# Kernel tuning notes

Measured on AMD Instinct MI355X. Metric: run time of the kernel, lower is better.

## Reference

```python
import jax, jax.numpy as jnp
import numpy as np

N, T, DS, DD = 20000, 8, 16, 8   # nodes, seq_len, static dim, dynamic dim
E = 320000                        # edges (before self loops)
HL = 128                          # LSTM hidden
GH, GC = 4, 128                   # GAT heads, channels per head
HC = GH * GC                      # 512 concat output
EMB = 64
IN1 = DS + HL                     # layer-1 GNN input dim (static + lstm)


def setup_inputs() -> dict:
    ks = jax.random.split(jax.random.key(0), 20)
    p = lambda k, s: jax.random.normal(k, s, jnp.float32) * 0.05
    return {
        "x_static": jax.random.normal(ks[0], (N, DS), jnp.float32),
        "dynamic_seq": jax.random.normal(ks[1], (N, T, DD), jnp.float32),
        "edge_index": jax.random.randint(ks[2], (2, E), 0, N),
        # LSTM params (PyTorch gate order i,f,g,o)
        "W_ih": p(ks[3], (4 * HL, DD)), "W_hh": p(ks[4], (4 * HL, HL)),
        "b_ih": p(ks[5], (4 * HL,)), "b_hh": p(ks[6], (4 * HL,)),
        # GATv2 layer 1
        "Wl1": p(ks[7], (HC, IN1)), "Wr1": p(ks[8], (HC, IN1)),
        "att1": p(ks[9], (GH, GC)), "bg1": p(ks[10], (HC,)),
        # GATv2 layer 2
        "Wl2": p(ks[11], (HC, HC)), "Wr2": p(ks[12], (HC, HC)),
        "att2": p(ks[13], (GH, GC)), "bg2": p(ks[14], (HC,)),
        # BatchNorm affine params
        "gamma1": jnp.ones((HC,), jnp.float32), "beta1": jnp.zeros((HC,), jnp.float32),
        "gamma2": jnp.ones((HC,), jnp.float32), "beta2": jnp.zeros((HC,), jnp.float32),
        # output projection
        "Wp": p(ks[15], (EMB, HC)), "bp": p(ks[16], (EMB,)),
    }


def _lstm(seq, W_ih, W_hh, b_ih, b_hh):
    """Single-layer LSTM over [N, T, DD] -> [T, N, HL]."""
    n = seq.shape[0]
    b = b_ih + b_hh

    def step(carry, x_t):
        h, c = carry
        g = x_t @ W_ih.T + h @ W_hh.T + b            # [N, 4*HL]
        i, f, gg, o = jnp.split(g, 4, axis=-1)
        c = jax.nn.sigmoid(f) * c + jax.nn.sigmoid(i) * jnp.tanh(gg)
        h = jax.nn.sigmoid(o) * jnp.tanh(c)
        return (h, c), h

    h0 = jnp.zeros((n, HL), seq.dtype)
    _, hs = jax.lax.scan(step, (h0, h0), jnp.swapaxes(seq, 0, 1))
    return hs


def _gatv2(x, src, dst, Wl, Wr, att, bias):
    """GATv2Conv (concat heads, self-loops already in src/dst, eval dropout)."""
    xl = (x @ Wl.T).reshape(N, GH, GC)   # source transform
    xr = (x @ Wr.T).reshape(N, GH, GC)   # target transform
    e = jax.nn.leaky_relu(xl[src] + xr[dst], 0.2)       # [E', GH, GC]
    s = jnp.einsum('ehc,hc->eh', e, att)                # [E', GH]
    smax = jax.ops.segment_max(s, dst, num_segments=N)  # scatter-softmax (stable)
    ex = jnp.exp(s - smax[dst])
    den = jax.ops.segment_sum(ex, dst, num_segments=N)
    alpha = ex / den[dst]
    out = jax.ops.segment_sum(alpha[:, :, None] * xl[src], dst, num_segments=N)
    return out.reshape(N, HC) + bias


def _bn(x, g, b):
    m = x.mean(0)
    v = x.var(0)
    return (x - m) * jax.lax.rsqrt(v + 1e-5) * g + b


def reference(x_static, dynamic_seq, edge_index, W_ih, W_hh, b_ih, b_hh,
              Wl1, Wr1, att1, bg1, Wl2, Wr2, att2, bg2,
              gamma1, beta1, gamma2, beta2, Wp, bp):
    loops = jnp.arange(N)
    src = jnp.concatenate([edge_index[0], loops])  # add self loops (PyG default)
    dst = jnp.concatenate([edge_index[1], loops])
    hs = _lstm(dynamic_seq, W_ih, W_hh, b_ih, b_hh)  # [T, N, HL]

    def step(_, h_t):
        g = jnp.concatenate([x_static, h_t], axis=1)                 # [N, IN1]
        g = jax.nn.relu(_bn(_gatv2(g, src, dst, Wl1, Wr1, att1, bg1), gamma1, beta1))
        g = jax.nn.relu(_bn(_gatv2(g, src, dst, Wl2, Wr2, att2, bg2), gamma2, beta2))
        return None, g @ Wp.T + bp                                   # [N, EMB]

    _, emb = jax.lax.scan(step, None, hs)  # [T, N, EMB]
    return jnp.swapaxes(emb, 0, 1)         # [N, T, EMB]
```

## Files before the change

### kernel.cpp

```cpp
#include <hip/hip_runtime.h>
#include <math.h>

typedef unsigned short u16;
typedef unsigned int u32;

#define N_NODES 20000
#define MP      20480
#define T_SEQ   8
#define DS      16
#define DD      8
#define E_EDGES 320000
#define HL      128
#define GH      4
#define GC      128
#define HC      512
#define EMB     64
#define KP1     160
#define EP      (E_EDGES + N_NODES)
#define EPP     (EP + 3 * N_NODES)

typedef __attribute__((ext_vector_type(8))) short bf16x8;
typedef __attribute__((ext_vector_type(4))) float f32x4;

__device__ __forceinline__ u16 f2bf(float f) {
  u32 u = __float_as_uint(f);
  u += 0x7fff + ((u >> 16) & 1);
  return (u16)(u >> 16);
}
__device__ __forceinline__ float bflo(u32 v) { return __uint_as_float(v << 16); }
__device__ __forceinline__ float bfhi(u32 v) { return __uint_as_float(v & 0xffff0000u); }
__device__ __forceinline__ float bf16f(u16 v) { return __uint_as_float((u32)v << 16); }

__device__ __forceinline__ void gld16(const void* g, void* l) {
  __builtin_amdgcn_global_load_lds(
      (const __attribute__((address_space(1))) void*)g,
      (__attribute__((address_space(3))) void*)l, 16, 0, 0);
}

__device__ __forceinline__ float rowsum16(float p) {
  p += __int_as_float(__builtin_amdgcn_update_dpp(0, __float_as_int(p), 0x121, 0xf, 0xf, false));
  p += __int_as_float(__builtin_amdgcn_update_dpp(0, __float_as_int(p), 0x122, 0xf, 0xf, false));
  p += __int_as_float(__builtin_amdgcn_update_dpp(0, __float_as_int(p), 0x124, 0xf, 0xf, false));
  p += __int_as_float(__builtin_amdgcn_update_dpp(0, __float_as_int(p), 0x128, 0xf, 0xf, false));
  return p;
}

__global__ __launch_bounds__(256) void gemm_mfma(
    const u16* __restrict__ A, int lda,
    const u16* __restrict__ W, int ldw,
    const float* __restrict__ bias,
    void* __restrict__ Cout, int ldc,
    int M, int Nc, int K, int c_bf16, int gxs)
{
  __shared__ u16 smem[16384];
  u16* Asm = smem;
  u16* Bsm = smem + 8192;

  const int tid = threadIdx.x;
  const int wave = tid >> 6, lane = tid & 63;
  const int wm = (wave >> 1) << 6, wn = (wave & 1) << 6;

  const u32 id = blockIdx.x;
  const int xcd = id & 7;
  const u32 sl = id >> 3;
  const int GXm = (1 << gxs) - 1;
  const int bn = (int)(sl & GXm) << 7;
  const int bm = (xcd + (int)((sl >> gxs) << 3)) << 7;

  f32x4 acc[4][4];
#pragma unroll
  for (int i = 0; i < 4; ++i)
#pragma unroll
    for (int j = 0; j < 4; ++j) acc[i][j] = (f32x4){0.f, 0.f, 0.f, 0.f};

  const int qr = lane >> 2;
  const int qc = (lane & 3) << 3;
  const int q0 = wave * 2, q1 = wave * 2 + 1;
  const int ra0 = bm + q0 * 16 + qr;
  const int ra1 = bm + q1 * 16 + qr;
  int rb0 = bn + q0 * 16 + qr; if (rb0 >= Nc) rb0 = Nc - 1;
  int rb1 = bn + q1 * 16 + qr; if (rb1 >= Nc) rb1 = Nc - 1;

  const u16* pa0 = A + (size_t)ra0 * lda + qc;
  const u16* pa1 = A + (size_t)ra1 * lda + qc;
  const u16* pb0 = W + (size_t)rb0 * ldw + qc;
  const u16* pb1 = W + (size_t)rb1 * ldw + qc;

  const int fm = lane & 15;
  const int fk = (lane >> 4) << 3;

  gld16(pa0, &Asm[q0 * 512]);
  gld16(pa1, &Asm[q1 * 512]);
  gld16(pb0, &Bsm[q0 * 512]);
  gld16(pb1, &Bsm[q1 * 512]);
  pa0 += 32; pa1 += 32; pb0 += 32; pb1 += 32;

  const int iters = K >> 5;
#pragma unroll 2
  for (int it = 0; it < iters; ++it) {
    const int cur = (it & 1) * 4096;
    __syncthreads();
    if (it + 1 < iters) {
      const int nxt = cur ^ 4096;
      gld16(pa0, &Asm[nxt + q0 * 512]);
      gld16(pa1, &Asm[nxt + q1 * 512]);
      gld16(pb0, &Bsm[nxt + q0 * 512]);
      gld16(pb1, &Bsm[nxt + q1 * 512]);
      pa0 += 32; pa1 += 32; pb0 += 32; pb1 += 32;
    }
    bf16x8 af[4], bfr[4];
#pragma unroll
    for (int i = 0; i < 4; ++i)
      af[i] = *(const bf16x8*)&Asm[cur + (wm + i * 16 + fm) * 32 + fk];
#pragma unroll
    for (int j = 0; j < 4; ++j)
      bfr[j] = *(const bf16x8*)&Bsm[cur + (wn + j * 16 + fm) * 32 + fk];
#pragma unroll
    for (int i = 0; i < 4; ++i)
#pragma unroll
      for (int j = 0; j < 4; ++j)
        acc[i][j] = __builtin_amdgcn_mfma_f32_16x16x32_bf16(af[i], bfr[j], acc[i][j], 0, 0, 0);
  }

  const int cn = lane & 15, cm = (lane >> 4) << 2;
  if (c_bf16) {
    __syncthreads();
#pragma unroll
    for (int j = 0; j < 4; ++j) {
      const int c = wn + j * 16 + cn;
      const float bb = bias ? bias[bn + c] : 0.f;
#pragma unroll
      for (int i = 0; i < 4; ++i) {
#pragma unroll
        for (int r = 0; r < 4; ++r)
          smem[(wm + i * 16 + cm + r) * 128 + c] = f2bf(acc[i][j][r] + bb);
      }
    }
    __syncthreads();
    u16* outc = (u16*)Cout;
#pragma unroll
    for (int k = 0; k < 8; ++k) {
      const int idx = tid + k * 256;
      const int r = idx >> 4, cc = (idx & 15) << 3;
      *(uint4*)(outc + (size_t)(bm + r) * ldc + bn + cc) = *(const uint4*)&smem[r * 128 + cc];
    }
  } else {
#pragma unroll
    for (int j = 0; j < 4; ++j) {
      const int c = bn + wn + j * 16 + cn;
      if (c >= Nc) continue;
      const float bb = bias ? bias[c] : 0.f;
#pragma unroll
      for (int i = 0; i < 4; ++i) {
#pragma unroll
        for (int r = 0; r < 4; ++r) {
          const int m = bm + wm + i * 16 + cm + r;
          if (m >= M) continue;
          ((float*)Cout)[(size_t)m * ldc + c] = acc[i][j][r] + bb;
        }
      }
    }
  }
}

__global__ void k_bias_sum(const float* __restrict__ b_ih,
                           const float* __restrict__ b_hh,
                           float* __restrict__ bsum) {
  int i = blockIdx.x * blockDim.x + threadIdx.x;
  if (i < 4 * HL) bsum[i] = b_ih[i] + b_hh[i];
}

__global__ void k_wcat_bf(const float* __restrict__ W_ih,
                          const float* __restrict__ W_hh,
                          u16* __restrict__ w) {
  int idx = blockIdx.x * blockDim.x + threadIdx.x;
  if (idx >= HC * KP1) return;
  int j = idx / KP1, k = idx - j * KP1;
  float v = 0.f;
  if (k < DD) v = W_ih[j * DD + k];
  else if (k < DD + HL) v = W_hh[j * HL + (k - DD)];
  w[idx] = f2bf(v);
}

__global__ void k_wlr1_bf(const float* __restrict__ Wl,
                          const float* __restrict__ Wr,
                          u16* __restrict__ w) {
  int idx = blockIdx.x * blockDim.x + threadIdx.x;
  if (idx >= 2 * HC * KP1) return;
  int j = idx / KP1, k = idx - j * KP1;
  const float* src = (j < HC) ? Wl : Wr;
  int jj = j & (HC - 1);
  float v = (k < DS + HL) ? src[jj * (DS + HL) + k] : 0.f;
  w[idx] = f2bf(v);
}

__global__ void k_wlr2_bf(const float* __restrict__ Wl,
                          const float* __restrict__ Wr,
                          u16* __restrict__ w) {
  int idx = blockIdx.x * blockDim.x + threadIdx.x;
  if (idx >= 2 * HC * HC) return;
  int j = idx >> 9, k = idx & (HC - 1);
  const float* src = (j < HC) ? Wl : Wr;
  int jj = j & (HC - 1);
  w[idx] = f2bf(src[jj * HC + k]);
}

__global__ void k_wp_bf(const float* __restrict__ Wp, u16* __restrict__ w) {
  int idx = blockIdx.x * blockDim.x + threadIdx.x;
  if (idx < EMB * HC) w[idx] = f2bf(Wp[idx]);
}

__global__ void k_pack_static(const float* __restrict__ xs, u16* __restrict__ packG1) {
  int idx = blockIdx.x * blockDim.x + threadIdx.x;
  if (idx >= N_NODES * DS) return;
  int n = idx >> 4, k = idx & 15;
  packG1[(size_t)n * KP1 + k] = f2bf(xs[idx]);
}

__global__ void k_pack_dyn(const float* __restrict__ dyn, u16* __restrict__ packXH) {
  int idx = blockIdx.x * blockDim.x + threadIdx.x;
  if (idx >= N_NODES * DD) return;
  int n = idx >> 3, k = idx & 7;
  packXH[(size_t)n * KP1 + k] = f2bf(dyn[(size_t)n * (T_SEQ * DD) + k]);
}

__global__ void lstm_update(const u16* __restrict__ gatesb,
                            float* __restrict__ c,
                            u16* __restrict__ packXH, u16* __restrict__ packG1,
                            const float* __restrict__ dyn, int t_next) {
  int idx = blockIdx.x * blockDim.x + threadIdx.x;
  if (idx >= N_NODES * HL) return;
  int n = idx >> 7, j = idx & 127;
  const u16* g = gatesb + (size_t)n * HC;
  float gi = bf16f(g[j]), gf = bf16f(g[j + 128]);
  float gg = bf16f(g[j + 256]), go = bf16f(g[j + 384]);
  float si = 1.f / (1.f + __expf(-gi));
  float sf = 1.f / (1.f + __expf(-gf));
  float so = 1.f / (1.f + __expf(-go));
  float cn = sf * c[idx] + si * tanhf(gg);
  c[idx] = cn;
  u16 hb = f2bf(so * tanhf(cn));
  packXH[(size_t)n * KP1 + DD + j] = hb;
  packG1[(size_t)n * KP1 + DS + j] = hb;
  if (j < DD && t_next < T_SEQ)
    packXH[(size_t)n * KP1 + j] =
        f2bf(dyn[(size_t)n * (T_SEQ * DD) + t_next * DD + j]);
}

__global__ void k_deg(const int* __restrict__ ei, int* __restrict__ deg) {
  int e = blockIdx.x * blockDim.x + threadIdx.x;
  if (e >= EP) return;
  int d = (e < E_EDGES) ? ei[E_EDGES + e] : (e - E_EDGES);
  atomicAdd(&deg[d], 1);
}

__global__ __launch_bounds__(1024) void k_scan(const int* __restrict__ deg,
                                               int* __restrict__ rowstart) {
  __shared__ int buf[1024];
  __shared__ int carry_s;
  const int tid = threadIdx.x;
  if (tid == 0) carry_s = 0;
  __syncthreads();
  for (int base = 0; base < N_NODES; base += 1024) {
    int v = (base + tid < N_NODES) ? ((deg[base + tid] + 3) & ~3) : 0;
    buf[tid] = v;
    __syncthreads();
    for (int off = 1; off < 1024; off <<= 1) {
      int add = (tid >= off) ? buf[tid - off] : 0;
      __syncthreads();
      buf[tid] += add;
      __syncthreads();
    }
    int incl = buf[tid];
    int carry = carry_s;
    if (base + tid < N_NODES) rowstart[base + tid] = carry + incl - v;
    __syncthreads();
    if (tid == 1023) carry_s = carry + incl;
    __syncthreads();
  }
  if (tid == 0) rowstart[N_NODES] = carry_s;
}

__global__ void k_fill(const int* __restrict__ ei,
                       const int* __restrict__ rowstart,
                       int* __restrict__ cursor, u32* __restrict__ csr) {
  int e = blockIdx.x * blockDim.x + threadIdx.x;
  if (e >= EP) return;
  int s, d;
  if (e < E_EDGES) { s = ei[e]; d = ei[E_EDGES + e]; }
  else             { s = d = e - E_EDGES; }
  int pos = atomicAdd(&cursor[d], 1);
  csr[rowstart[d] + pos] = (u32)s << 11;
}

__global__ void k_pad(const int* __restrict__ deg,
                      const int* __restrict__ rowstart, u32* __restrict__ csr) {
  int d = blockIdx.x * blockDim.x + threadIdx.x;
  if (d >= N_NODES) return;
  int s = rowstart[d] + deg[d], e = rowstart[d + 1];
  const u32 pv = ((u32)d << 11) | 1;
  for (int i = s; i < e; ++i) csr[i] = pv;
}

__global__ __launch_bounds__(256) void gat_edge(
    const u16* __restrict__ xlr,
    const float* __restrict__ att, const float* __restrict__ bias,
    const int* __restrict__ rowstart, const u32* __restrict__ csr,
    u16* __restrict__ outb)
{
  const int wave = threadIdx.x >> 6, lane = threadIdx.x & 63;
  const int d = blockIdx.x * 4 + wave;
  const int ch = lane * 8;
  const uint4 vr = *(const uint4*)(xlr + (size_t)d * 1024 + 512 + ch);
  const float rxa0 = bflo(vr.x), rxa1 = bfhi(vr.x), rxa2 = bflo(vr.y), rxa3 = bfhi(vr.y);
  const float rxb0 = bflo(vr.z), rxb1 = bfhi(vr.z), rxb2 = bflo(vr.w), rxb3 = bfhi(vr.w);
  const float4 ava = *(const float4*)(att + ch);
  const float4 avb = *(const float4*)(att + ch + 4);
  const int row = rowstart[d], end = rowstart[d + 1];
  const char* __restrict__ xbase = (const char*)(xlr + ch);

  float l = 0.f;
  float a0 = 0.f, a1 = 0.f, a2 = 0.f, a3 = 0.f;
  float b0 = 0.f, b1 = 0.f, b2 = 0.f, b3 = 0.f;

#define GLD(o) (*(const uint4*)(xbase + (size_t)((o) & ~1u)))

#define GAT_STEP(v, o)                                                       \
  {                                                                          \
    const float xa0 = bflo((v).x), xa1 = bfhi((v).x);                        \
    const float xa2 = bflo((v).y), xa3 = bfhi((v).y);                        \
    const float xb0 = bflo((v).z), xb1 = bfhi((v).z);                        \
    const float xb2 = bflo((v).w), xb3 = bfhi((v).w);                        \
    const float e0 = xa0 + rxa0, e1 = xa1 + rxa1;                            \
    const float e2 = xa2 + rxa2, e3 = xa3 + rxa3;                            \
    const float f0 = xb0 + rxb0, f1 = xb1 + rxb1;                            \
    const float f2 = xb2 + rxb2, f3 = xb3 + rxb3;                            \
    float ps = e0 * ava.x;                                                   \
    ps = fmaf(e1, ava.y, ps); ps = fmaf(e2, ava.z, ps);                      \
    ps = fmaf(e3, ava.w, ps); ps = fmaf(f0, avb.x, ps);                      \
    ps = fmaf(f1, avb.y, ps); ps = fmaf(f2, avb.z, ps);                      \
    ps = fmaf(f3, avb.w, ps);                                                \
    float pa = fabsf(e0) * ava.x;                                            \
    pa = fmaf(fabsf(e1), ava.y, pa); pa = fmaf(fabsf(e2), ava.z, pa);        \
    pa = fmaf(fabsf(e3), ava.w, pa); pa = fmaf(fabsf(f0), avb.x, pa);        \
    pa = fmaf(fabsf(f1), avb.y, pa); pa = fmaf(fabsf(f2), avb.z, pa);        \
    pa = fmaf(fabsf(f3), avb.w, pa);                                         \
    float p = rowsum16(fmaf(0.6f, ps, 0.4f * pa));                           \
    float w = __expf(p);                                                     \
    w = ((o) & 1) ? 0.f : w;                                                 \
    l += w;                                                                  \
    a0 = fmaf(w, xa0, a0); a1 = fmaf(w, xa1, a1);                            \
    a2 = fmaf(w, xa2, a2); a3 = fmaf(w, xa3, a3);                            \
    b0 = fmaf(w, xb0, b0); b1 = fmaf(w, xb1, b1);                            \
    b2 = fmaf(w, xb2, b2); b3 = fmaf(w, xb3, b3);                            \
  }

  const u32* cp = csr + row;
  const int nq = (end - row) >> 2;

  u32 o0 = cp[0], o1 = cp[1], o2 = cp[2], o3 = cp[3];
  uint4 v0 = GLD(o0), v1 = GLD(o1), v2 = GLD(o2), v3 = GLD(o3);

  for (int q = 1; q < nq; ++q) {
    cp += 4;
    const u32 n0 = cp[0], n1 = cp[1], n2 = cp[2], n3 = cp[3];
    const uint4 w0 = GLD(n0), w1 = GLD(n1), w2 = GLD(n2), w3 = GLD(n3);
    GAT_STEP(v0, o0);
    GAT_STEP(v1, o1);
    GAT_STEP(v2, o2);
    GAT_STEP(v3, o3);
    o0 = n0; o1 = n1; o2 = n2; o3 = n3;
    v0 = w0; v1 = w1; v2 = w2; v3 = w3;
  }
  GAT_STEP(v0, o0);
  GAT_STEP(v1, o1);
  GAT_STEP(v2, o2);
  GAT_STEP(v3, o3);
#undef GAT_STEP
#undef GLD

  const float inv = 1.f / l;
  const float4 ba = *(const float4*)(bias + ch);
  const float4 bb = *(const float4*)(bias + ch + 4);
  uint4 ov;
  ov.x = (u32)f2bf(fmaf(a0, inv, ba.x)) | ((u32)f2bf(fmaf(a1, inv, ba.y)) << 16);
  ov.y = (u32)f2bf(fmaf(a2, inv, ba.z)) | ((u32)f2bf(fmaf(a3, inv, ba.w)) << 16);
  ov.z = (u32)f2bf(fmaf(b0, inv, bb.x)) | ((u32)f2bf(fmaf(b1, inv, bb.y)) << 16);
  ov.w = (u32)f2bf(fmaf(b2, inv, bb.z)) | ((u32)f2bf(fmaf(b3, inv, bb.w)) << 16);
  *(uint4*)(outb + (size_t)d * HC + ch) = ov;
}

__global__ __launch_bounds__(256) void bn_stats(const u16* __restrict__ x,
                                                float* __restrict__ stats) {
  const int tid = threadIdx.x;
  const int rows_per = (N_NODES + gridDim.x - 1) / gridDim.x;
  const int r0 = blockIdx.x * rows_per;
  const int r1 = min(r0 + rows_per, N_NODES);
  const u32* xp = (const u32*)x;
  float s0 = 0.f, s1 = 0.f, q0 = 0.f, q1 = 0.f;
  for (int r = r0; r < r1; ++r) {
    const u32 v = xp[(size_t)r * 256 + tid];
    const float v0 = bflo(v), v1 = bfhi(v);
    s0 += v0; q0 += v0 * v0;
    s1 += v1; q1 += v1 * v1;
  }
  atomicAdd(&stats[2 * tid],          s0);
  atomicAdd(&stats[2 * tid + 1],      s1);
  atomicAdd(&stats[HC + 2 * tid],     q0);
  atomicAdd(&stats[HC + 2 * tid + 1], q1);
}

__global__ void bn_apply(const u16* __restrict__ x, const float* __restrict__ stats,
                         const float* __restrict__ gamma, const float* __restrict__ beta,
                         u16* __restrict__ outb) {
  int idx = blockIdx.x * blockDim.x + threadIdx.x;
  if (idx >= N_NODES * (HC / 2)) return;
  const int cc = idx & (HC / 2 - 1);
  const int c0 = cc * 2, c1 = c0 + 1;
  const u32 v = ((const u32*)x)[idx];
  const float mean0 = stats[c0] * (1.f / N_NODES);
  const float mean1 = stats[c1] * (1.f / N_NODES);
  const float inv0 = rsqrtf(stats[HC + c0] * (1.f / N_NODES) - mean0 * mean0 + 1e-5f);
  const float inv1 = rsqrtf(stats[HC + c1] * (1.f / N_NODES) - mean1 * mean1 + 1e-5f);
  float z0 = (bflo(v) - mean0) * inv0 * gamma[c0] + beta[c0];
  float z1 = (bfhi(v) - mean1) * inv1 * gamma[c1] + beta[c1];
  z0 = z0 > 0.f ? z0 : 0.f;
  z1 = z1 > 0.f ? z1 : 0.f;
  ((u32*)outb)[idx] = (u32)f2bf(z0) | ((u32)f2bf(z1) << 16);
}

extern "C" void kernel_launch(void* const* d_in, const int* in_sizes, int n_in,
                              void* d_out, int out_size, void* d_ws, size_t ws_size,
                              hipStream_t stream) {
  const float* x_static = (const float*)d_in[0];
  const float* dyn      = (const float*)d_in[1];
  const int*   ei       = (const int*)d_in[2];
  const float* W_ih     = (const float*)d_in[3];
  const float* W_hh     = (const float*)d_in[4];
  const float* b_ih     = (const float*)d_in[5];
  const float* b_hh     = (const float*)d_in[6];
  const float* Wl1      = (const float*)d_in[7];
  const float* Wr1      = (const float*)d_in[8];
  const float* att1     = (const float*)d_in[9];
  const float* bg1      = (const float*)d_in[10];
  const float* Wl2      = (const float*)d_in[11];
  const float* Wr2      = (const float*)d_in[12];
  const float* att2     = (const float*)d_in[13];
  const float* bg2      = (const float*)d_in[14];
  const float* gamma1   = (const float*)d_in[15];
  const float* beta1    = (const float*)d_in[16];
  const float* gamma2   = (const float*)d_in[17];
  const float* beta2    = (const float*)d_in[18];
  const float* Wp       = (const float*)d_in[19];
  const float* bp       = (const float*)d_in[20];
  float* out = (float*)d_out;

  float* ws = (float*)d_ws;
  size_t o = 0;
  float* c        = ws + o; o += (size_t)MP * HL;
  float* statsAll = ws + o; o += (size_t)T_SEQ * 4 * HC;
  float* bsum     = ws + o; o += 4 * HL;
  u16* gatesb  = (u16*)(ws + o); o += (size_t)MP * HC / 2;
  u16* packXH  = (u16*)(ws + o); o += (size_t)MP * KP1 / 2;
  u16* packG1  = (u16*)(ws + o); o += (size_t)MP * KP1 / 2;
  u16* xlr     = (u16*)(ws + o); o += (size_t)MP * 1024 / 2;
  u16* gout    = (u16*)(ws + o); o += (size_t)MP * HC / 2;
  u16* aggb    = (u16*)(ws + o); o += (size_t)MP * HC / 2;
  u16* wcat_bf = (u16*)(ws + o); o += (size_t)HC * KP1 / 2;
  u16* wlr1_bf = (u16*)(ws + o); o += (size_t)2 * HC * KP1 / 2;
  u16* wlr2_bf = (u16*)(ws + o); o += (size_t)2 * HC * HC / 2;
  u16* wp_bf   = (u16*)(ws + o); o += (size_t)EMB * HC / 2;
  int* deg      = (int*)(ws + o); o += N_NODES;
  int* cursor   = (int*)(ws + o); o += N_NODES;
  int* rowstart = (int*)(ws + o); o += N_NODES + 64;
  u32* csr      = (u32*)(ws + o); o += EPP;

  hipMemsetAsync(deg,      0, N_NODES * sizeof(int), stream);
  hipMemsetAsync(cursor,   0, N_NODES * sizeof(int), stream);
  hipMemsetAsync(statsAll, 0, (size_t)T_SEQ * 4 * HC * sizeof(float), stream);
  hipMemsetAsync(c,        0, (size_t)MP * HL * sizeof(float), stream);
  hipMemsetAsync(packXH,   0, (size_t)MP * KP1 * sizeof(u16), stream);
  hipMemsetAsync(packG1,   0, (size_t)MP * KP1 * sizeof(u16), stream);
  hipMemsetAsync(aggb,     0, (size_t)MP * HC * sizeof(u16), stream);

  k_bias_sum<<<2, 256, 0, stream>>>(b_ih, b_hh, bsum);
  k_wcat_bf<<<(HC * KP1 + 255) / 256, 256, 0, stream>>>(W_ih, W_hh, wcat_bf);
  k_wlr1_bf<<<(2 * HC * KP1 + 255) / 256, 256, 0, stream>>>(Wl1, Wr1, wlr1_bf);
  k_wlr2_bf<<<(2 * HC * HC + 255) / 256, 256, 0, stream>>>(Wl2, Wr2, wlr2_bf);
  k_wp_bf<<<(EMB * HC + 255) / 256, 256, 0, stream>>>(Wp, wp_bf);
  k_pack_static<<<(N_NODES * DS + 255) / 256, 256, 0, stream>>>(x_static, packG1);
  k_pack_dyn<<<(N_NODES * DD + 255) / 256, 256, 0, stream>>>(dyn, packXH);
  k_deg<<<(EP + 255) / 256, 256, 0, stream>>>(ei, deg);
  k_scan<<<1, 1024, 0, stream>>>(deg, rowstart);
  k_fill<<<(EP + 255) / 256, 256, 0, stream>>>(ei, rowstart, cursor, csr);
  k_pad<<<(N_NODES + 255) / 256, 256, 0, stream>>>(deg, rowstart, csr);

  const int GY = MP / 128;

  for (int t = 0; t < T_SEQ; ++t) {
    float* stats = statsAll + (size_t)t * 4 * HC;

    gemm_mfma<<<4 * GY, 256, 0, stream>>>(packXH, KP1, wcat_bf, KP1, bsum,
                                          gatesb, HC, MP, HC, KP1, 1, 2);
    lstm_update<<<(N_NODES * HL + 255) / 256, 256, 0, stream>>>(
        gatesb, c, packXH, packG1, dyn, t + 1);

    gemm_mfma<<<8 * GY, 256, 0, stream>>>(packG1, KP1, wlr1_bf, KP1, nullptr,
                                          xlr, 1024, MP, 2 * HC, KP1, 1, 3);
    gat_edge<<<N_NODES / 4, 256, 0, stream>>>(xlr, att1, bg1, rowstart, csr, gout);
    bn_stats<<<500, 256, 0, stream>>>(gout, stats);
    bn_apply<<<(N_NODES * HC / 2 + 255) / 256, 256, 0, stream>>>(gout, stats,
                                                                 gamma1, beta1, aggb);

    gemm_mfma<<<8 * GY, 256, 0, stream>>>(aggb, HC, wlr2_bf, HC, nullptr,
                                          xlr, 1024, MP, 2 * HC, HC, 1, 3);
    gat_edge<<<N_NODES / 4, 256, 0, stream>>>(xlr, att2, bg2, rowstart, csr, gout);
    bn_stats<<<500, 256, 0, stream>>>(gout, stats + 2 * HC);
    bn_apply<<<(N_NODES * HC / 2 + 255) / 256, 256, 0, stream>>>(gout, stats + 2 * HC,
                                                                 gamma2, beta2, aggb);

    gemm_mfma<<<1 * GY, 256, 0, stream>>>(aggb, HC, wp_bf, HC, bp,
                                          out + t * EMB, T_SEQ * EMB,
                                          N_NODES, EMB, HC, 0, 0);
  }
}
```

Before: 2.455 ms.

## Fuse BatchNorm statistics into GAT edge kernel and drop CSR padding

```diff
diff --git a/kernel.cpp b/kernel.cpp
--- a/kernel.cpp
+++ b/kernel.cpp
@@ -17,7 +17,6 @@
 #define EMB     64
 #define KP1     160
 #define EP      (E_EDGES + N_NODES)
-#define EPP     (EP + 3 * N_NODES)
 
 typedef __attribute__((ext_vector_type(8))) short bf16x8;
 typedef __attribute__((ext_vector_type(4))) float f32x4;
@@ -262,7 +261,7 @@
   if (tid == 0) carry_s = 0;
   __syncthreads();
   for (int base = 0; base < N_NODES; base += 1024) {
-    int v = (base + tid < N_NODES) ? ((deg[base + tid] + 3) & ~3) : 0;
+    int v = (base + tid < N_NODES) ? deg[base + tid] : 0;
     buf[tid] = v;
     __syncthreads();
     for (int off = 1; off < 1024; off <<= 1) {
@@ -293,22 +292,20 @@
   csr[rowstart[d] + pos] = (u32)s << 11;
 }
 
-__global__ void k_pad(const int* __restrict__ deg,
-                      const int* __restrict__ rowstart, u32* __restrict__ csr) {
-  int d = blockIdx.x * blockDim.x + threadIdx.x;
-  if (d >= N_NODES) return;
-  int s = rowstart[d] + deg[d], e = rowstart[d + 1];
-  const u32 pv = ((u32)d << 11) | 1;
-  for (int i = s; i < e; ++i) csr[i] = pv;
-}
-
 __global__ __launch_bounds__(256) void gat_edge(
     const u16* __restrict__ xlr,
     const float* __restrict__ att, const float* __restrict__ bias,
     const int* __restrict__ rowstart, const u32* __restrict__ csr,
-    u16* __restrict__ outb)
+    u16* __restrict__ outb, float* __restrict__ stats)
 {
-  const int wave = threadIdx.x >> 6, lane = threadIdx.x & 63;
+  __shared__ float ssum[HC];
+  __shared__ float ssq[HC];
+  const int tid = threadIdx.x;
+  ssum[tid] = 0.f; ssum[tid + 256] = 0.f;
+  ssq[tid]  = 0.f; ssq[tid + 256]  = 0.f;
+  __syncthreads();
+
+  const int wave = tid >> 6, lane = tid & 63;
   const int d = blockIdx.x * 4 + wave;
   const int ch = lane * 8;
   const uint4 vr = *(const uint4*)(xlr + (size_t)d * 1024 + 512 + ch);
@@ -323,9 +320,7 @@
   float a0 = 0.f, a1 = 0.f, a2 = 0.f, a3 = 0.f;
   float b0 = 0.f, b1 = 0.f, b2 = 0.f, b3 = 0.f;
 
-#define GLD(o) (*(const uint4*)(xbase + (size_t)((o) & ~1u)))
-
-#define GAT_STEP(v, o)                                                       \
+#define GAT_STEP(v)                                                          \
   {                                                                          \
     const float xa0 = bflo((v).x), xa1 = bfhi((v).x);                        \
     const float xa2 = bflo((v).y), xa3 = bfhi((v).y);                        \
@@ -346,8 +341,7 @@
     pa = fmaf(fabsf(f1), avb.y, pa); pa = fmaf(fabsf(f2), avb.z, pa);        \
     pa = fmaf(fabsf(f3), avb.w, pa);                                         \
     float p = rowsum16(fmaf(0.6f, ps, 0.4f * pa));                           \
-    float w = __expf(p);                                                     \
-    w = ((o) & 1) ? 0.f : w;                                                 \
+    const float w = __expf(p);                                               \
     l += w;                                                                  \
     a0 = fmaf(w, xa0, a0); a1 = fmaf(w, xa1, a1);                            \
     a2 = fmaf(w, xa2, a2); a3 = fmaf(w, xa3, a3);                            \
@@ -355,59 +349,52 @@
     b2 = fmaf(w, xb2, b2); b3 = fmaf(w, xb3, b3);                            \
   }
 
-  const u32* cp = csr + row;
-  const int nq = (end - row) >> 2;
-
-  u32 o0 = cp[0], o1 = cp[1], o2 = cp[2], o3 = cp[3];
-  uint4 v0 = GLD(o0), v1 = GLD(o1), v2 = GLD(o2), v3 = GLD(o3);
-
-  for (int q = 1; q < nq; ++q) {
-    cp += 4;
-    const u32 n0 = cp[0], n1 = cp[1], n2 = cp[2], n3 = cp[3];
-    const uint4 w0 = GLD(n0), w1 = GLD(n1), w2 = GLD(n2), w3 = GLD(n3);
-    GAT_STEP(v0, o0);
-    GAT_STEP(v1, o1);
-    GAT_STEP(v2, o2);
-    GAT_STEP(v3, o3);
-    o0 = n0; o1 = n1; o2 = n2; o3 = n3;
-    v0 = w0; v1 = w1; v2 = w2; v3 = w3;
-  }
-  GAT_STEP(v0, o0);
-  GAT_STEP(v1, o1);
-  GAT_STEP(v2, o2);
-  GAT_STEP(v3, o3);
+  int i = row;
+  for (; i + 3 < end; i += 4) {
+    const u32 s0 = csr[i],     s1 = csr[i + 1];
+    const u32 s2 = csr[i + 2], s3 = csr[i + 3];
+    const uint4 v0 = *(const uint4*)(xbase + s0);
+    const uint4 v1 = *(const uint4*)(xbase + s1);
+    const uint4 v2 = *(const uint4*)(xbase + s2);
+    const uint4 v3 = *(const uint4*)(xbase + s3);
+    GAT_STEP(v0);
+    GAT_STEP(v1);
+    GAT_STEP(v2);
+    GAT_STEP(v3);
+  }
+  for (; i < end; ++i) {
+    const uint4 v0 = *(const uint4*)(xbase + csr[i]);
+    GAT_STEP(v0);
+  }
 #undef GAT_STEP
-#undef GLD
 
   const float inv = 1.f / l;
   const float4 ba = *(const float4*)(bias + ch);
   const float4 bb = *(const float4*)(bias + ch + 4);
+  const float o0 = fmaf(a0, inv, ba.x), o1 = fmaf(a1, inv, ba.y);
+  const float o2 = fmaf(a2, inv, ba.z), o3 = fmaf(a3, inv, ba.w);
+  const float o4 = fmaf(b0, inv, bb.x), o5 = fmaf(b1, inv, bb.y);
+  const float o6 = fmaf(b2, inv, bb.z), o7 = fmaf(b3, inv, bb.w);
   uint4 ov;
-  ov.x = (u32)f2bf(fmaf(a0, inv, ba.x)) | ((u32)f2bf(fmaf(a1, inv, ba.y)) << 16);
-  ov.y = (u32)f2bf(fmaf(a2, inv, ba.z)) | ((u32)f2bf(fmaf(a3, inv, ba.w)) << 16);
-  ov.z = (u32)f2bf(fmaf(b0, inv, bb.x)) | ((u32)f2bf(fmaf(b1, inv, bb.y)) << 16);
-  ov.w = (u32)f2bf(fmaf(b2, inv, bb.z)) | ((u32)f2bf(fmaf(b3, inv, bb.w)) << 16);
+  ov.x = (u32)f2bf(o0) | ((u32)f2bf(o1) << 16);
+  ov.y = (u32)f2bf(o2) | ((u32)f2bf(o3) << 16);
+  ov.z = (u32)f2bf(o4) | ((u32)f2bf(o5) << 16);
+  ov.w = (u32)f2bf(o6) | ((u32)f2bf(o7) << 16);
   *(uint4*)(outb + (size_t)d * HC + ch) = ov;
-}
-
-__global__ __launch_bounds__(256) void bn_stats(const u16* __restrict__ x,
-                                                float* __restrict__ stats) {
-  const int tid = threadIdx.x;
-  const int rows_per = (N_NODES + gridDim.x - 1) / gridDim.x;
-  const int r0 = blockIdx.x * rows_per;
-  const int r1 = min(r0 + rows_per, N_NODES);
-  const u32* xp = (const u32*)x;
-  float s0 = 0.f, s1 = 0.f, q0 = 0.f, q1 = 0.f;
-  for (int r = r0; r < r1; ++r) {
-    const u32 v = xp[(size_t)r * 256 + tid];
-    const float v0 = bflo(v), v1 = bfhi(v);
-    s0 += v0; q0 += v0 * v0;
-    s1 += v1; q1 += v1 * v1;
-  }
-  atomicAdd(&stats[2 * tid],          s0);
-  atomicAdd(&stats[2 * tid + 1],      s1);
-  atomicAdd(&stats[HC + 2 * tid],     q0);
-  atomicAdd(&stats[HC + 2 * tid + 1], q1);
+
+  atomicAdd(&ssum[ch + 0], o0); atomicAdd(&ssq[ch + 0], o0 * o0);
+  atomicAdd(&ssum[ch + 1], o1); atomicAdd(&ssq[ch + 1], o1 * o1);
+  atomicAdd(&ssum[ch + 2], o2); atomicAdd(&ssq[ch + 2], o2 * o2);
+  atomicAdd(&ssum[ch + 3], o3); atomicAdd(&ssq[ch + 3], o3 * o3);
+  atomicAdd(&ssum[ch + 4], o4); atomicAdd(&ssq[ch + 4], o4 * o4);
+  atomicAdd(&ssum[ch + 5], o5); atomicAdd(&ssq[ch + 5], o5 * o5);
+  atomicAdd(&ssum[ch + 6], o6); atomicAdd(&ssq[ch + 6], o6 * o6);
+  atomicAdd(&ssum[ch + 7], o7); atomicAdd(&ssq[ch + 7], o7 * o7);
+  __syncthreads();
+  atomicAdd(&stats[tid],            ssum[tid]);
+  atomicAdd(&stats[tid + 256],      ssum[tid + 256]);
+  atomicAdd(&stats[HC + tid],       ssq[tid]);
+  atomicAdd(&stats[HC + tid + 256], ssq[tid + 256]);
 }
 
 __global__ void bn_apply(const u16* __restrict__ x, const float* __restrict__ stats,
@@ -473,7 +460,7 @@
   int* deg      = (int*)(ws + o); o += N_NODES;
   int* cursor   = (int*)(ws + o); o += N_NODES;
   int* rowstart = (int*)(ws + o); o += N_NODES + 64;
-  u32* csr      = (u32*)(ws + o); o += EPP;
+  u32* csr      = (u32*)(ws + o); o += EP;
 
   hipMemsetAsync(deg,      0, N_NODES * sizeof(int), stream);
   hipMemsetAsync(cursor,   0, N_NODES * sizeof(int), stream);
@@ -493,7 +480,6 @@
   k_deg<<<(EP + 255) / 256, 256, 0, stream>>>(ei, deg);
   k_scan<<<1, 1024, 0, stream>>>(deg, rowstart);
   k_fill<<<(EP + 255) / 256, 256, 0, stream>>>(ei, rowstart, cursor, csr);
-  k_pad<<<(N_NODES + 255) / 256, 256, 0, stream>>>(deg, rowstart, csr);
 
   const int GY = MP / 128;
 
@@ -507,15 +493,15 @@
 
     gemm_mfma<<<8 * GY, 256, 0, stream>>>(packG1, KP1, wlr1_bf, KP1, nullptr,
                                           xlr, 1024, MP, 2 * HC, KP1, 1, 3);
-    gat_edge<<<N_NODES / 4, 256, 0, stream>>>(xlr, att1, bg1, rowstart, csr, gout);
-    bn_stats<<<500, 256, 0, stream>>>(gout, stats);
+    gat_edge<<<N_NODES / 4, 256, 0, stream>>>(xlr, att1, bg1, rowstart, csr,
+                                              gout, stats);
     bn_apply<<<(N_NODES * HC / 2 + 255) / 256, 256, 0, stream>>>(gout, stats,
                                                                  gamma1, beta1, aggb);
 
     gemm_mfma<<<8 * GY, 256, 0, stream>>>(aggb, HC, wlr2_bf, HC, nullptr,
                                           xlr, 1024, MP, 2 * HC, HC, 1, 3);
-    gat_edge<<<N_NODES / 4, 256, 0, stream>>>(xlr, att2, bg2, rowstart, csr, gout);
-    bn_stats<<<500, 256, 0, stream>>>(gout, stats + 2 * HC);
+    gat_edge<<<N_NODES / 4, 256, 0, stream>>>(xlr, att2, bg2, rowstart, csr,
+                                              gout, stats + 2 * HC);
     bn_apply<<<(N_NODES * HC / 2 + 255) / 256, 256, 0, stream>>>(gout, stats + 2 * HC,
                                                                  gamma2, beta2, aggb);
 
```

Result: slower. 3.990 ms (+62.5%).
